# Optimization experiments

Hardware: AMD Instinct MI355X
Metric: run time of the kernel (lower is better)

Reference implementation:

```python
import jax, jax.numpy as jnp
import numpy as np

N, T, D, H = 128, 64, 1024, 1024
DA = 4  # spatial dim of feature map


def setup_inputs() -> dict:
    key = jax.random.key(0)
    k1, k2, k3, k4, k5 = jax.random.split(key, 5)
    x = jax.random.normal(k1, (N, T, D), dtype=jnp.float32)
    A = jax.random.normal(k2, (N, H, DA, DA), dtype=jnp.float32)
    Wx = jax.random.normal(k3, (D, 4 * H), dtype=jnp.float32) / np.sqrt(D)
    Wh = jax.random.normal(k4, (H, 4 * H), dtype=jnp.float32) / np.sqrt(H)
    Wattn = jax.random.normal(k5, (H, 4 * H), dtype=jnp.float32) / np.sqrt(H)
    b = jnp.zeros((4 * H,), dtype=jnp.float32)
    return {"x": x, "A": A, "Wx": Wx, "Wh": Wh, "Wattn": Wattn, "b": b}


def _dot_product_attention(prev_h, A_flat):
    # prev_h: (N, H), A_flat: (N, H, L) with L = DA*DA
    scores = jnp.einsum('nh,nhl->nl', prev_h, A_flat) / jnp.sqrt(jnp.float32(H))
    w = jax.nn.softmax(scores, axis=-1)              # (N, L)
    attn = jnp.einsum('nhl,nl->nh', A_flat, w)       # (N, H)
    return attn


def reference(x, A, Wx, Wh, Wattn, b):
    A_flat = A.reshape(A.shape[0], A.shape[1], -1)   # (N, H, L)
    h0 = A.mean(axis=(2, 3))                          # (N, H)
    c0 = h0
    x_t = jnp.swapaxes(x, 0, 1)                       # (T, N, D)

    def step(carry, xt):
        h, c = carry
        attn = _dot_product_attention(h, A_flat)
        a = xt @ Wx + h @ Wh + attn @ Wattn + b       # (N, 4H)
        i, f, o, g = jnp.split(a, 4, axis=1)
        i = jax.nn.sigmoid(i)
        f = jax.nn.sigmoid(f)
        o = jax.nn.sigmoid(o)
        g = jnp.tanh(g)
        c_next = f * c + i * g
        h_next = o * jnp.tanh(c_next)
        return (h_next, c_next), h_next

    _, hn = jax.lax.scan(step, (h0, c0), x_t)         # hn: (T, N, H)
    return jnp.swapaxes(hn, 0, 1)                      # (N, T, H)
```

## Files before the change

### kernel.cpp

```cpp
#include <hip/hip_runtime.h>
#include <stdint.h>
#include <math.h>

typedef __attribute__((ext_vector_type(8))) short short8;
typedef __attribute__((ext_vector_type(4))) short short4v;
typedef __attribute__((ext_vector_type(4))) float f32x4;

__device__ __forceinline__ short f2bf(float f){
  union { float f; uint32_t u; } x; x.f = f;
  uint32_t r = x.u + 0x7fffu + ((x.u >> 16) & 1u);
  return (short)(r >> 16);
}
__device__ __forceinline__ float bf2f(short s){
  union { uint32_t u; float f; } x; x.u = ((uint32_t)(uint16_t)s) << 16;
  return x.f;
}

__device__ __forceinline__ unsigned ld_llc_u32(const void* p){
  return __hip_atomic_load((const unsigned*)p, __ATOMIC_RELAXED, __HIP_MEMORY_SCOPE_AGENT);
}
__device__ __forceinline__ void st_llc_u32(void* p, unsigned v){
  __hip_atomic_store((unsigned*)p, v, __ATOMIC_RELAXED, __HIP_MEMORY_SCOPE_AGENT);
}


__global__ __launch_bounds__(256) void k_wt(const float* __restrict__ Wx,
                                            const float* __restrict__ Wh,
                                            const float* __restrict__ Wattn,
                                            short* __restrict__ W3T){
  __shared__ float tile[64][65];
  int bk = blockIdx.x % 48, bj = blockIdx.x / 48;
  int tx = threadIdx.x & 63, ty = threadIdx.x >> 6;
  int k0 = bk * 64, j0 = bj * 64;
  #pragma unroll
  for (int i = 0; i < 16; ++i){
    int kk = ty * 16 + i;
    int k = k0 + kk;
    const float* src = (k < 1024) ? (Wx + (size_t)k * 4096)
                     : (k < 2048) ? (Wh + (size_t)(k - 1024) * 4096)
                                  : (Wattn + (size_t)(k - 2048) * 4096);
    tile[kk][tx] = src[j0 + tx];
  }
  __syncthreads();
  #pragma unroll
  for (int i = 0; i < 16; ++i){
    int jj = ty * 16 + i;
    W3T[(size_t)(j0 + jj) * 3072 + k0 + tx] = f2bf(tile[tx][jj]);
  }
}

__global__ __launch_bounds__(256) void k_cast(const float* __restrict__ in,
                                              short* __restrict__ out, int n4){
  int i = blockIdx.x * 256 + threadIdx.x;
  if (i >= n4) return;
  float4 v = ((const float4*)in)[i];
  short4v o; o[0] = f2bf(v.x); o[1] = f2bf(v.y); o[2] = f2bf(v.z); o[3] = f2bf(v.w);
  *(short4v*)(out + (size_t)i * 4) = o;
}

__global__ __launch_bounds__(256) void k_castA(const float* __restrict__ A,
                                               short* __restrict__ Abf,
                                               short* __restrict__ Atr){
  const int n = blockIdx.x;
  const int tid = threadIdx.x;
  __shared__ short tile[256][17];
  for (int it = 0; it < 4; ++it){
    int h = it * 256 + tid;
    const float* src = A + ((size_t)n * 1024 + h) * 16;
    short o[16];
    #pragma unroll
    for (int l = 0; l < 16; ++l) o[l] = f2bf(src[l]);
    short8 p0, p1;
    #pragma unroll
    for (int l = 0; l < 8; ++l){ p0[l] = o[l]; p1[l] = o[8 + l]; }
    short8* dst = (short8*)(Abf + ((size_t)n * 1024 + h) * 16);
    dst[0] = p0; dst[1] = p1;
    #pragma unroll
    for (int l = 0; l < 16; ++l) tile[tid][l] = o[l];
    __syncthreads();
    {
      int l = tid >> 4, hc = (tid & 15) * 16;
      short tmp[16];
      #pragma unroll
      for (int k = 0; k < 16; ++k) tmp[k] = tile[hc + k][l];
      short8 q0, q1;
      #pragma unroll
      for (int k = 0; k < 8; ++k){ q0[k] = tmp[k]; q1[k] = tmp[8 + k]; }
      short8* d2 = (short8*)(Atr + (size_t)n * 16384 + l * 1024 + it * 256 + hc);
      d2[0] = q0; d2[1] = q1;
    }
    __syncthreads();
  }
}

__global__ __launch_bounds__(256) void k_init(const float* __restrict__ A,
                                              float* __restrict__ c,
                                              short* __restrict__ hb0,
                                              unsigned* __restrict__ flags){
  int idx = blockIdx.x * 256 + threadIdx.x;
  if (idx < 8192) flags[idx] = 0u;
  const float* p = A + (size_t)idx * 16;
  float s = 0.f;
  #pragma unroll
  for (int l = 0; l < 16; ++l) s += p[l];
  s *= (1.f / 16.f);
  c[idx] = s;
  hb0[idx] = f2bf(s);
}

typedef const __attribute__((address_space(1))) uint32_t* gas1_t;
typedef __attribute__((address_space(3))) uint32_t* las3_t;

__global__ __launch_bounds__(256) void k_xwx(const short* __restrict__ xbf,
                                             const short* __restrict__ W3T,
                                             short* __restrict__ xwx){
  __shared__ short ldsA[128 * 64];
  __shared__ short ldsB[128 * 64];
  const int tid  = threadIdx.x;
  const int lane = tid & 63;
  const int wave = tid >> 6;
  const int orig = blockIdx.x;
  const int wg = (orig & 7) * 256 + (orig >> 3);
  const int n_t = wg >> 6;
  const int m_t = wg & 63;
  const int m0 = m_t * 128;
  const int n0 = n_t * 128;
  const int ra = lane & 15;
  const int q  = lane >> 4;

  f32x4 acc[4][4];
  #pragma unroll
  for (int mf = 0; mf < 4; ++mf)
    #pragma unroll
    for (int jf = 0; jf < 4; ++jf) acc[mf][jf] = f32x4{0.f,0.f,0.f,0.f};

  const int wm = wave >> 1;
  const int wn = wave & 1;

  for (int kt = 0; kt < 16; ++kt){
    const int kb = kt * 64;
    #pragma unroll
    for (int r = 0; r < 4; ++r){
      int id = (wave * 4 + r) * 64 + lane;
      int row = id >> 3, c = id & 7;
      int csrc = c ^ (row & 7);
      const short* src = xbf + (size_t)(m0 + row) * 1024 + kb + csrc * 8;
      short* dst = ldsA + (wave * 4 + r) * 512;
      __builtin_amdgcn_global_load_lds((gas1_t)(const void*)src, (las3_t)(void*)dst, 16, 0, 0);
    }
    #pragma unroll
    for (int r = 0; r < 4; ++r){
      int id = (wave * 4 + r) * 64 + lane;
      int row = id >> 3, c = id & 7;
      int csrc = c ^ (row & 7);
      const short* src = W3T + (size_t)(n0 + row) * 3072 + kb + csrc * 8;
      short* dst = ldsB + (wave * 4 + r) * 512;
      __builtin_amdgcn_global_load_lds((gas1_t)(const void*)src, (las3_t)(void*)dst, 16, 0, 0);
    }
    asm volatile("s_waitcnt vmcnt(0)" ::: "memory");
    __syncthreads();

    #pragma unroll
    for (int kk = 0; kk < 64; kk += 32){
      const int cc = (kk >> 3) + q;
      short8 af[4], bfr[4];
      #pragma unroll
      for (int mf = 0; mf < 4; ++mf){
        int row = wm * 64 + mf * 16 + ra;
        af[mf] = *(const short8*)(ldsA + row * 64 + ((cc ^ (row & 7)) << 3));
      }
      #pragma unroll
      for (int jf = 0; jf < 4; ++jf){
        int row = wn * 64 + jf * 16 + ra;
        bfr[jf] = *(const short8*)(ldsB + row * 64 + ((cc ^ (row & 7)) << 3));
      }
      #pragma unroll
      for (int mf = 0; mf < 4; ++mf)
        #pragma unroll
        for (int jf = 0; jf < 4; ++jf)
          acc[mf][jf] = __builtin_amdgcn_mfma_f32_16x16x32_bf16(af[mf], bfr[jf], acc[mf][jf], 0, 0, 0);
    }
    __syncthreads();
  }

  #pragma unroll
  for (int mf = 0; mf < 4; ++mf)
    #pragma unroll
    for (int jf = 0; jf < 4; ++jf)
      #pragma unroll
      for (int i = 0; i < 4; ++i){
        int row = m0 + wm * 64 + mf * 16 + q * 4 + i;
        int col = n0 + wn * 64 + jf * 16 + ra;
        xwx[(size_t)row * 4096 + col] = f2bf(acc[mf][jf][i]);
      }
}

__global__ __launch_bounds__(256) void k_pw(const short* __restrict__ W3T,
                                            const short* __restrict__ Atr,
                                            short* __restrict__ P){
  const int tid  = threadIdx.x;
  const int lane = tid & 63;
  const int wave = tid >> 6;
  const int blk  = blockIdx.x;
  const int n    = blk >> 4;
  const int jblk = blk & 15;
  const int j0   = jblk * 256 + wave * 64;
  const int ra = lane & 15;
  const int q  = lane >> 4;

  f32x4 acc[4];
  #pragma unroll
  for (int mf = 0; mf < 4; ++mf) acc[mf] = f32x4{0.f,0.f,0.f,0.f};

  auto loadA = [&](int ks, int mf) -> short8 {
    return *(const short8*)(W3T + (size_t)(j0 + mf*16 + ra) * 3072 + 2048 + ks * 32 + q * 8);
  };
  auto loadB = [&](int ks) -> short8 {
    return *(const short8*)(Atr + (size_t)n * 16384 + ra * 1024 + ks * 32 + q * 8);
  };

  short8 aC[4], bC, aN[4], bN;
  #pragma unroll
  for (int mf = 0; mf < 4; ++mf) aC[mf] = loadA(0, mf);
  bC = loadB(0);
  for (int ks = 0; ks < 32; ++ks){
    bool more = (ks + 1) < 32;
    if (more){
      #pragma unroll
      for (int mf = 0; mf < 4; ++mf) aN[mf] = loadA(ks + 1, mf);
      bN = loadB(ks + 1);
    }
    #pragma unroll
    for (int mf = 0; mf < 4; ++mf)
      acc[mf] = __builtin_amdgcn_mfma_f32_16x16x32_bf16(aC[mf], bC, acc[mf], 0, 0, 0);
    if (more){
      #pragma unroll
      for (int mf = 0; mf < 4; ++mf) aC[mf] = aN[mf];
      bC = bN;
    }
  }
  #pragma unroll
  for (int mf = 0; mf < 4; ++mf)
    #pragma unroll
    for (int i = 0; i < 4; ++i){
      int j = j0 + mf * 16 + q * 4 + i;
      P[(size_t)(n * 4096 + j) * 16 + ra] = f2bf(acc[mf][i]);
    }
}

__global__ __launch_bounds__(512, 1) void k_loop(
    const short* __restrict__ W3T,
    const short* __restrict__ Abf,
    const short* __restrict__ P,
    short* __restrict__ hbuf,
    float* __restrict__ wbuf,
    const float* __restrict__ cbuf,
    const short* __restrict__ xwx,
    const float* __restrict__ bias,
    float* __restrict__ out,
    unsigned* __restrict__ flags)
{
  __shared__ short Wl[32768];
  __shared__ float redu[4096];
  __shared__ float sred[4][16];
  __shared__ float wlds[64][16];

  unsigned* flagsB = flags;
  unsigned* wtag   = flags + 4096;

  const int tid  = threadIdx.x;
  const int lane = tid & 63;
  const int wave = tid >> 6;
  const int bid  = blockIdx.x;
  const int mh   = bid & 1;
  const int jb   = bid >> 1;
  const int u0   = jb * 8;
  const int ra   = lane & 15;
  const int q    = lane >> 4;
  const int mf2  = wave & 1;
  const int kh   = wave >> 1;
  const bool isScore = (bid < 128);
  const int n_s  = mh * 64 + jb;
  const bool doScore = (wave < 4) && isScore;

  #pragma unroll
  for (int it = 0; it < 8; ++it){
    int c16 = it * 512 + tid;
    int jl = c16 >> 7;
    int kc = c16 & 127;
    int jf = jl >> 4, rr = jl & 15;
    int j = (jf * 2 + (rr >> 3)) * 1024 + u0 + (rr & 7);
    short8 v = *(const short8*)(W3T + (size_t)j * 3072 + 1024 + kc * 8);
    int pc = (jf * 16 + rr) * 128 + (kc ^ (rr & 7));
    *(short8*)(Wl + pc * 8) = v;
  }

  const int n_loc = tid >> 3, uu = tid & 7;
  const int cn = mh * 64 + n_loc;
  const int cu = u0 + uu;
  float creg = cbuf[(size_t)cn * 1024 + cu];
  const float b0 = bias[cu], b1 = bias[1024 + cu], b2 = bias[2048 + cu], b3 = bias[3072 + cu];
  short8 pA[4], pB[4];
  #pragma unroll
  for (int g = 0; g < 4; ++g){
    const short8* pp = (const short8*)(P + ((size_t)cn * 4096 + g * 1024 + cu) * 16);
    pA[g] = pp[0]; pB[g] = pp[1];
  }
  const int hh0 = tid * 4;
  __syncthreads();

  for (int t = 0; t < 64; ++t){
    const short* hRp = hbuf + (size_t)t * 131072;
    short*       hWp = hbuf + (size_t)(t + 1) * 131072;
    float*       wT  = wbuf + (size_t)t * 4096;

    const short* xp = xwx + ((size_t)cn * 64 + t) * 4096;
    const short xw0 = xp[cu], xw1 = xp[1024 + cu], xw2 = xp[2048 + cu], xw3 = xp[3072 + cu];

    if (t > 0){
      if (wave == 0){
        const unsigned tgt = (unsigned)t;
        for (;;){
          unsigned v0 = ld_llc_u32(&flagsB[(mh * 128 + lane * 2)     * 16]);
          unsigned v1 = ld_llc_u32(&flagsB[(mh * 128 + lane * 2 + 1) * 16]);
          unsigned mn = v0 < v1 ? v0 : v1;
          if (__all(mn >= tgt)) break;
          __builtin_amdgcn_s_sleep(2);
        }
      }
      __syncthreads();
    }

    auto loadA = [&](int ks, int m) -> short8 {
      const int kk = kh * 256 + ks * 32 + q * 8;
      const int row = mh * 64 + mf2 * 32 + m * 16 + ra;
      return *(const short8*)(hRp + row * 1024 + kk);
    };
    auto loadB = [&](int ks, int jf) -> short8 {
      const int kcg = kh * 32 + ks * 4 + q;
      const int sw = kcg ^ (ra & 7);
      return *(const short8*)(Wl + (((jf * 16 + ra) * 128) + sw) * 8);
    };

    short8 Ab[4][2];
    if (!doScore){
      #pragma unroll
      for (int p = 0; p < 4; ++p){ Ab[p][0] = loadA(p, 0); Ab[p][1] = loadA(p, 1); }
    }

    if (doScore){
      short8 af0[4], af1[4];
      #pragma unroll
      for (int j = 0; j < 4; ++j){
        const short8* ap = (const short8*)(Abf + ((size_t)n_s * 1024 + hh0 + j) * 16);
        af0[j] = ap[0]; af1[j] = ap[1];
      }
      uint64_t hq = *(const uint64_t*)(hRp + n_s * 1024 + hh0);
      float hv[4];
      #pragma unroll
      for (int j = 0; j < 4; ++j) hv[j] = bf2f((short)((hq >> (16 * j)) & 0xffffu));
      float sc[16];
      #pragma unroll
      for (int l = 0; l < 8; ++l){
        float s0 = 0.f, s1 = 0.f;
        #pragma unroll
        for (int j = 0; j < 4; ++j){ s0 += hv[j] * bf2f(af0[j][l]); s1 += hv[j] * bf2f(af1[j][l]); }
        sc[l] = s0; sc[8 + l] = s1;
      }
      #pragma unroll
      for (int off = 1; off < 64; off <<= 1)
        #pragma unroll
        for (int l = 0; l < 16; ++l) sc[l] += __shfl_xor(sc[l], off);
      if (lane == 0)
        #pragma unroll
        for (int l = 0; l < 16; ++l) sred[wave][l] = sc[l];
    }
    __syncthreads();

    if (wave == 0 && isScore){
      float s[16], mx = -1e30f, sum = 0.f;
      #pragma unroll
      for (int l = 0; l < 16; ++l){
        s[l] = (sred[0][l] + sred[1][l] + sred[2][l] + sred[3][l]) * 0.03125f;
        mx = fmaxf(mx, s[l]);
      }
      #pragma unroll
      for (int l = 0; l < 16; ++l){ s[l] = __expf(s[l] - mx); sum += s[l]; }
      const float inv = 1.f / sum;
      #pragma unroll
      for (int l = 0; l < 16; ++l){
        if (lane == l){
          union { float f; unsigned u; } cv; cv.f = s[l] * inv;
          st_llc_u32(&wT[n_s * 32 + l], cv.u);
        }
      }
      asm volatile("s_waitcnt vmcnt(0)" ::: "memory");
      if (lane == 0) st_llc_u32(&wtag[n_s * 16], (unsigned)(t + 1));
    }

    if (doScore){
      #pragma unroll
      for (int p = 0; p < 4; ++p){ Ab[p][0] = loadA(p, 0); Ab[p][1] = loadA(p, 1); }
    }
    short8 Bb[2][2];
    Bb[0][0] = loadB(0, 0); Bb[0][1] = loadB(0, 1);
    Bb[1][0] = loadB(1, 0); Bb[1][1] = loadB(1, 1);

    f32x4 acc[2][2];
    acc[0][0] = f32x4{0.f,0.f,0.f,0.f}; acc[0][1] = f32x4{0.f,0.f,0.f,0.f};
    acc[1][0] = f32x4{0.f,0.f,0.f,0.f}; acc[1][1] = f32x4{0.f,0.f,0.f,0.f};

    #pragma unroll
    for (int ks = 0; ks < 8; ++ks){
      short8 av0 = Ab[ks & 3][0], av1 = Ab[ks & 3][1];
      short8 bv0 = Bb[ks & 1][0], bv1 = Bb[ks & 1][1];
      if (ks < 4){ Ab[ks & 3][0] = loadA(ks + 4, 0); Ab[ks & 3][1] = loadA(ks + 4, 1); }
      if (ks < 6){ Bb[ks & 1][0] = loadB(ks + 2, 0); Bb[ks & 1][1] = loadB(ks + 2, 1); }
      acc[0][0] = __builtin_amdgcn_mfma_f32_16x16x32_bf16(av0, bv0, acc[0][0], 0, 0, 0);
      acc[0][1] = __builtin_amdgcn_mfma_f32_16x16x32_bf16(av0, bv1, acc[0][1], 0, 0, 0);
      acc[1][0] = __builtin_amdgcn_mfma_f32_16x16x32_bf16(av1, bv0, acc[1][0], 0, 0, 0);
      acc[1][1] = __builtin_amdgcn_mfma_f32_16x16x32_bf16(av1, bv1, acc[1][1], 0, 0, 0);
    }

    auto ridx = [&](int m2, int khq, int m, int jf) -> float* {
      return &redu[((((m2 * 2 + khq) * 2 + m) * 2 + jf) * 64 + lane) * 4];
    };
    if (kh & 1){
      *(f32x4*)ridx(mf2, kh >> 1, 0, 0) = acc[0][0];
      *(f32x4*)ridx(mf2, kh >> 1, 0, 1) = acc[0][1];
      *(f32x4*)ridx(mf2, kh >> 1, 1, 0) = acc[1][0];
      *(f32x4*)ridx(mf2, kh >> 1, 1, 1) = acc[1][1];
    }
    __syncthreads();
    if (!(kh & 1)){
      acc[0][0] += *(const f32x4*)ridx(mf2, kh >> 1, 0, 0);
      acc[0][1] += *(const f32x4*)ridx(mf2, kh >> 1, 0, 1);
      acc[1][0] += *(const f32x4*)ridx(mf2, kh >> 1, 1, 0);
      acc[1][1] += *(const f32x4*)ridx(mf2, kh >> 1, 1, 1);
    }
    if (wave == 2){
      const unsigned tgt = (unsigned)(t + 1);
      for (;;){
        unsigned v = ld_llc_u32(&wtag[(mh * 64 + lane) * 16]);
        if (__all(v >= tgt)) break;
        __builtin_amdgcn_s_sleep(2);
      }
      const f32x4* wp = (const f32x4*)(wT + (mh * 64 + lane) * 32);
      f32x4 w0 = wp[0], w1 = wp[1], w2 = wp[2], w3 = wp[3];
      f32x4* wd = (f32x4*)&wlds[lane][0];
      wd[0] = w0; wd[1] = w1; wd[2] = w2; wd[3] = w3;
    }
    __syncthreads();
    if (kh == 2){
      *(f32x4*)ridx(mf2, 0, 0, 0) = acc[0][0];
      *(f32x4*)ridx(mf2, 0, 0, 1) = acc[0][1];
      *(f32x4*)ridx(mf2, 0, 1, 0) = acc[1][0];
      *(f32x4*)ridx(mf2, 0, 1, 1) = acc[1][1];
    }
    __syncthreads();
    if (kh == 0){
      acc[0][0] += *(const f32x4*)ridx(mf2, 0, 0, 0);
      acc[0][1] += *(const f32x4*)ridx(mf2, 0, 0, 1);
      acc[1][0] += *(const f32x4*)ridx(mf2, 0, 1, 0);
      acc[1][1] += *(const f32x4*)ridx(mf2, 0, 1, 1);
    }
    __syncthreads();
    if (kh == 0){
      #pragma unroll
      for (int m = 0; m < 2; ++m)
        #pragma unroll
        for (int jf = 0; jf < 2; ++jf){
          const int g = jf * 2 + (ra >> 3);
          const int nl = mf2 * 32 + m * 16 + q * 4;
          #pragma unroll
          for (int i = 0; i < 4; ++i)
            redu[g * 640 + (nl + i) * 10 + (ra & 7)] = acc[m][jf][i];
        }
    }
    __syncthreads();

    float hn;
    {
      float wl[16];
      #pragma unroll
      for (int l = 0; l < 16; ++l) wl[l] = wlds[n_loc][l];
      float pg[4];
      #pragma unroll
      for (int g = 0; g < 4; ++g){
        float s = 0.f;
        #pragma unroll
        for (int l = 0; l < 8; ++l){ s += bf2f(pA[g][l]) * wl[l]; s += bf2f(pB[g][l]) * wl[8 + l]; }
        pg[g] = s;
      }
      const int fb = n_loc * 10 + uu;
      const float av = redu[fb]         + bf2f(xw0) + pg[0] + b0;
      const float fv = redu[640 + fb]   + bf2f(xw1) + pg[1] + b1;
      const float ov = redu[1280 + fb]  + bf2f(xw2) + pg[2] + b2;
      const float gv = redu[1920 + fb]  + bf2f(xw3) + pg[3] + b3;
      const float ig = 1.f / (1.f + __expf(-av));
      const float fg = 1.f / (1.f + __expf(-fv));
      const float og = 1.f / (1.f + __expf(-ov));
      const float gcl = fminf(fmaxf(gv, -20.f), 20.f);
      const float e2g = __expf(2.f * gcl);
      const float gg = (e2g - 1.f) / (e2g + 1.f);
      creg = fg * creg + ig * gg;
      const float ccl = fminf(fmaxf(creg, -20.f), 20.f);
      const float e2c = __expf(2.f * ccl);
      const float th = (e2c - 1.f) / (e2c + 1.f);
      hn = og * th;
      const float hn2 = __shfl_xor(hn, 1);
      if ((tid & 1) == 0){
        unsigned pk = (unsigned)(unsigned short)f2bf(hn)
                    | ((unsigned)(unsigned short)f2bf(hn2) << 16);
        st_llc_u32(hWp + (size_t)cn * 1024 + cu, pk);
      }
    }
    asm volatile("s_waitcnt vmcnt(0)" ::: "memory");
    __syncthreads();
    if (tid == 0 && t < 63) st_llc_u32(&flagsB[(mh * 128 + jb) * 16], (unsigned)(t + 1));
    __builtin_nontemporal_store(hn, &out[((size_t)cn * 64 + t) * 1024 + cu]);
  }
}


extern "C" void kernel_launch(void* const* d_in, const int* in_sizes, int n_in,
                              void* d_out, int out_size, void* d_ws, size_t ws_size,
                              hipStream_t stream)
{
  const float* x     = (const float*)d_in[0];
  const float* A     = (const float*)d_in[1];
  const float* Wx    = (const float*)d_in[2];
  const float* Wh    = (const float*)d_in[3];
  const float* Wattn = (const float*)d_in[4];
  const float* b     = (const float*)d_in[5];
  float* out = (float*)d_out;
  char* ws = (char*)d_ws;

  short*    W3T   = (short*)(ws + 0);
  short*    Abf   = (short*)(ws + 25165824);
  short*    Atr   = (short*)(ws + 29360128);
  short*    xbf   = (short*)(ws + 33554432);
  short*    xwx   = (short*)(ws + 50331648);
  short*    P     = (short*)(ws + 117440512);
  short*    hbuf  = (short*)(ws + 134217728);
  float*    wbuf  = (float*)(ws + 151257088);
  float*    cbuf  = (float*)(ws + 152305664);
  unsigned* flags = (unsigned*)(ws + 152829952);

  hipLaunchKernelGGL(k_wt,    dim3(48 * 64), dim3(256), 0, stream, Wx, Wh, Wattn, W3T);
  hipLaunchKernelGGL(k_cast,  dim3(2097152 / 256), dim3(256), 0, stream, x, xbf, 2097152);
  hipLaunchKernelGGL(k_castA, dim3(128), dim3(256), 0, stream, A, Abf, Atr);
  hipLaunchKernelGGL(k_init,  dim3(512), dim3(256), 0, stream, A, cbuf, hbuf, flags);
  hipLaunchKernelGGL(k_xwx,   dim3(2048), dim3(256), 0, stream, xbf, W3T, xwx);
  hipLaunchKernelGGL(k_pw,    dim3(2048), dim3(256), 0, stream, W3T, Atr, P);
  hipLaunchKernelGGL(k_loop,  dim3(256), dim3(512), 0, stream,
                     W3T, Abf, P, hbuf, wbuf, cbuf, xwx, b, out, flags);
}
```

Baseline: 802.2 us.

## Use per-wave atomic flag increments and relayout xWx for coalesced per-block reads

Drops the block-wide barrier before publishing each step's h-ready flag. Each wave now waits for its own stores and atomically increments the block's flag, and consumers wait for a count of 8 per step. Separately, the precomputed x@Wx buffer is rewritten in a slot-major layout so each block reads one contiguous chunk per step, and the redundant reduction barrier is removed by writing to a separate redu region. The cost is eight atomics per block per step and a more intricate layout contract between the two kernels.

```diff
diff --git a/kernel.cpp b/kernel.cpp
--- a/kernel.cpp
+++ b/kernel.cpp
@@ -191,7 +191,11 @@
       for (int i = 0; i < 4; ++i){
         int row = m0 + wm * 64 + mf * 16 + q * 4 + i;
         int col = n0 + wn * 64 + jf * 16 + ra;
-        xwx[(size_t)row * 4096 + col] = f2bf(acc[mf][jf][i]);
+        int n = row >> 6, t = row & 63;
+        int g = col >> 10, cu = col & 1023;
+        int slot = ((n >> 6) & 1) * 128 + (cu >> 3);
+        size_t addr = ((size_t)(t * 256 + slot)) * 2048 + (n & 63) * 32 + g * 8 + (cu & 7);
+        xwx[addr] = f2bf(acc[mf][jf][i]);
       }
 }
 
@@ -261,7 +265,7 @@
     unsigned* __restrict__ flags)
 {
   __shared__ short Wl[32768];
-  __shared__ float redu[4096];
+  __shared__ float redu[4608];
   __shared__ float sred[4][16];
   __shared__ float wlds[64][16];
 
@@ -282,6 +286,7 @@
   const bool isScore = (bid < 128);
   const int n_s  = mh * 64 + jb;
   const bool doScore = (wave < 4) && isScore;
+  const int slot = mh * 128 + jb;
 
   #pragma unroll
   for (int it = 0; it < 8; ++it){
@@ -314,12 +319,12 @@
     short*       hWp = hbuf + (size_t)(t + 1) * 131072;
     float*       wT  = wbuf + (size_t)t * 4096;
 
-    const short* xp = xwx + ((size_t)cn * 64 + t) * 4096;
-    const short xw0 = xp[cu], xw1 = xp[1024 + cu], xw2 = xp[2048 + cu], xw3 = xp[3072 + cu];
+    const short* xp = xwx + ((size_t)(t * 256 + slot)) * 2048 + n_loc * 32 + uu;
+    const short xw0 = xp[0], xw1 = xp[8], xw2 = xp[16], xw3 = xp[24];
 
     if (t > 0){
       if (wave == 0){
-        const unsigned tgt = (unsigned)t;
+        const unsigned tgt = (unsigned)(8 * t);
         for (;;){
           unsigned v0 = ld_llc_u32(&flagsB[(mh * 128 + lane * 2)     * 16]);
           unsigned v1 = ld_llc_u32(&flagsB[(mh * 128 + lane * 2 + 1) * 16]);
@@ -463,9 +468,6 @@
       acc[0][1] += *(const f32x4*)ridx(mf2, 0, 0, 1);
       acc[1][0] += *(const f32x4*)ridx(mf2, 0, 1, 0);
       acc[1][1] += *(const f32x4*)ridx(mf2, 0, 1, 1);
-    }
-    __syncthreads();
-    if (kh == 0){
       #pragma unroll
       for (int m = 0; m < 2; ++m)
         #pragma unroll
@@ -474,7 +476,7 @@
           const int nl = mf2 * 32 + m * 16 + q * 4;
           #pragma unroll
           for (int i = 0; i < 4; ++i)
-            redu[g * 640 + (nl + i) * 10 + (ra & 7)] = acc[m][jf][i];
+            redu[2048 + g * 640 + (nl + i) * 10 + (ra & 7)] = acc[m][jf][i];
         }
     }
     __syncthreads();
@@ -493,10 +495,10 @@
         pg[g] = s;
       }
       const int fb = n_loc * 10 + uu;
-      const float av = redu[fb]         + bf2f(xw0) + pg[0] + b0;
-      const float fv = redu[640 + fb]   + bf2f(xw1) + pg[1] + b1;
-      const float ov = redu[1280 + fb]  + bf2f(xw2) + pg[2] + b2;
-      const float gv = redu[1920 + fb]  + bf2f(xw3) + pg[3] + b3;
+      const float av = redu[2048 + fb]        + bf2f(xw0) + pg[0] + b0;
+      const float fv = redu[2048 + 640 + fb]  + bf2f(xw1) + pg[1] + b1;
+      const float ov = redu[2048 + 1280 + fb] + bf2f(xw2) + pg[2] + b2;
+      const float gv = redu[2048 + 1920 + fb] + bf2f(xw3) + pg[3] + b3;
       const float ig = 1.f / (1.f + __expf(-av));
       const float fg = 1.f / (1.f + __expf(-fv));
       const float og = 1.f / (1.f + __expf(-ov));
@@ -515,9 +517,12 @@
         st_llc_u32(hWp + (size_t)cn * 1024 + cu, pk);
       }
     }
-    asm volatile("s_waitcnt vmcnt(0)" ::: "memory");
-    __syncthreads();
-    if (tid == 0 && t < 63) st_llc_u32(&flagsB[(mh * 128 + jb) * 16], (unsigned)(t + 1));
+    if (t < 63){
+      asm volatile("s_waitcnt vmcnt(0)" ::: "memory");
+      if (lane == 0)
+        __hip_atomic_fetch_add(&flagsB[(mh * 128 + jb) * 16], 1u,
+                               __ATOMIC_RELAXED, __HIP_MEMORY_SCOPE_AGENT);
+    }
     __builtin_nontemporal_store(hn, &out[((size_t)cn * 64 + t) * 1024 + cu]);
   }
 }
```

Measured after the change: 976.4 us. +21.7%, slower.
